# Kernel tuning notes

Measured on AMD Instinct MI355X. Metric: run time of the kernel, lower is better.

## Reference

```python
import jax, jax.numpy as jnp
import numpy as np

EMBED_DIM = 512
NUM_HEADS = 16
TGT_LEN = 1024
BSZ = 4
HEAD_DIM = EMBED_DIM // NUM_HEADS


def setup_inputs() -> dict:
    key = jax.random.key(0)
    ks = jax.random.split(key, 12)
    E = EMBED_DIM
    s = 1.0 / np.sqrt(E)
    query = jax.random.normal(ks[0], (TGT_LEN, BSZ, E), dtype=jnp.float32)
    attn_bias = jax.random.normal(ks[1], (BSZ * NUM_HEADS, TGT_LEN, TGT_LEN), dtype=jnp.float32)
    key_padding_mask = jax.random.randint(ks[2], (BSZ, TGT_LEN), 0, 2) == 1
    q_w = jax.random.normal(ks[3], (E, E), dtype=jnp.float32) * s
    q_b = jax.random.normal(ks[4], (E,), dtype=jnp.float32) * 0.02
    k_w = jax.random.normal(ks[5], (E, E), dtype=jnp.float32) * s
    k_b = jax.random.normal(ks[6], (E,), dtype=jnp.float32) * 0.02
    v_w = jax.random.normal(ks[7], (E, E), dtype=jnp.float32) * s
    v_b = jax.random.normal(ks[8], (E,), dtype=jnp.float32) * 0.02
    out_w = jax.random.normal(ks[9], (E, E), dtype=jnp.float32) * s
    out_b = jax.random.normal(ks[10], (E,), dtype=jnp.float32) * 0.02
    return {
        "query": query, "attn_bias": attn_bias, "key_padding_mask": key_padding_mask,
        "q_w": q_w, "q_b": q_b, "k_w": k_w, "k_b": k_b,
        "v_w": v_w, "v_b": v_b, "out_w": out_w, "out_b": out_b,
    }


def reference(query, attn_bias, key_padding_mask, q_w, q_b, k_w, k_b, v_w, v_b, out_w, out_b):
    Tlen, B, E = query.shape
    H, hd = NUM_HEADS, HEAD_DIM
    scaling = hd ** -0.5
    # self-attention: q/k/v all from query (Linear uses y = x @ W.T + b)
    q = (query @ q_w.T + q_b) * scaling
    k = query @ k_w.T + k_b
    v = query @ v_w.T + v_b
    # [T, B, E] -> [B*H, T, hd]
    q = q.reshape(Tlen, B * H, hd).transpose(1, 0, 2)
    k = k.reshape(Tlen, B * H, hd).transpose(1, 0, 2)
    v = v.reshape(Tlen, B * H, hd).transpose(1, 0, 2)
    # scores [B*H, T, S]
    aw = jnp.einsum('bth,bsh->bts', q, k) + attn_bias
    # key padding mask: [B, S] -> broadcast over heads and tgt
    aw = aw.reshape(B, H, Tlen, Tlen)
    aw = jnp.where(key_padding_mask[:, None, None, :], -jnp.inf, aw)
    aw = aw.reshape(B * H, Tlen, Tlen)
    probs = jax.nn.softmax(aw.astype(jnp.float32), axis=-1)
    attn = jnp.einsum('bts,bsh->bth', probs.astype(query.dtype), v)
    attn = attn.transpose(1, 0, 2).reshape(Tlen, B, E)
    out = attn @ out_w.T + out_b
    # need_weights=True, need_head_weights=False -> mean over heads, [B, T, S]
    attn_weights_avg = probs.reshape(B, H, Tlen, Tlen).mean(axis=1)
    return out, attn_weights_avg
```

## Files before the change

### kernel.cpp

```cpp
#include <hip/hip_runtime.h>
#include <math.h>

typedef __bf16 bf16x8 __attribute__((ext_vector_type(8)));
typedef __bf16 bf16x4 __attribute__((ext_vector_type(4)));
typedef float  f32x4  __attribute__((ext_vector_type(4)));

__global__ __launch_bounds__(256)
void cvt_w(const float* __restrict__ w0, const float* __restrict__ w1,
           const float* __restrict__ w2, const float* __restrict__ w3,
           __bf16* __restrict__ d0, __bf16* __restrict__ d1,
           __bf16* __restrict__ d2, __bf16* __restrict__ d3)
{
    const int y = blockIdx.y;
    const float* s = (y == 0) ? w0 : (y == 1) ? w1 : (y == 2) ? w2 : w3;
    __bf16*      d = (y == 0) ? d0 : (y == 1) ? d1 : (y == 2) ? d2 : d3;
    const int i = blockIdx.x * 256 + threadIdx.x;
    float4 a = *(const float4*)(s + (size_t)i * 8);
    float4 b = *(const float4*)(s + (size_t)i * 8 + 4);
    bf16x8 v;
    v[0] = (__bf16)a.x; v[1] = (__bf16)a.y; v[2] = (__bf16)a.z; v[3] = (__bf16)a.w;
    v[4] = (__bf16)b.x; v[5] = (__bf16)b.y; v[6] = (__bf16)b.z; v[7] = (__bf16)b.w;
    *(bf16x8*)(d + (size_t)i * 8) = v;
}

__global__ __launch_bounds__(256, 2)
void qkv_proj(const float* __restrict__ X,
              const __bf16* __restrict__ Wqb, const __bf16* __restrict__ Wkb,
              const __bf16* __restrict__ Wvb,
              const float* __restrict__ bq, const float* __restrict__ bk,
              const float* __restrict__ bv,
              __bf16* __restrict__ qTb, __bf16* __restrict__ kTb,
              __bf16* __restrict__ vTb)
{
    const int tid  = threadIdx.x;
    const int w    = tid >> 6;
    const int lane = tid & 63;
    const int lq   = lane & 15;
    const int quad = lane >> 4;
    const int n0    = blockIdx.x * 64 + (w >> 1) * 32;
    const int obase = blockIdx.y * 128 + (w & 1) * 64;

    const __bf16* const Wz[3] = { Wqb, Wkb, Wvb };

    f32x4 acc[3][2][4] = {};
    for (int k0 = 0; k0 < 512; k0 += 32) {
        bf16x8 af[2];
#pragma unroll
        for (int m = 0; m < 2; m++) {
            const float* xp = X + (size_t)(n0 + m * 16 + lq) * 512 + k0 + quad * 8;
            float4 x0 = *(const float4*)xp;
            float4 x1 = *(const float4*)(xp + 4);
            bf16x8 v;
            v[0] = (__bf16)x0.x; v[1] = (__bf16)x0.y; v[2] = (__bf16)x0.z; v[3] = (__bf16)x0.w;
            v[4] = (__bf16)x1.x; v[5] = (__bf16)x1.y; v[6] = (__bf16)x1.z; v[7] = (__bf16)x1.w;
            af[m] = v;
        }
#pragma unroll
        for (int z = 0; z < 3; z++) {
            bf16x8 bfr[4];
#pragma unroll
            for (int nn = 0; nn < 4; nn++)
                bfr[nn] = *(const bf16x8*)(Wz[z] + (size_t)(obase + nn * 16 + lq) * 512 + k0 + quad * 8);
#pragma unroll
            for (int m = 0; m < 2; m++)
#pragma unroll
                for (int nn = 0; nn < 4; nn++)
                    acc[z][m][nn] = __builtin_amdgcn_mfma_f32_16x16x32_bf16(af[m], bfr[nn], acc[z][m][nn], 0, 0, 0);
        }
    }

    const float* const ba[3] = { bq, bk, bv };
    const float scaling = 0.17677669529663687f;
#pragma unroll
    for (int z = 0; z < 3; z++)
#pragma unroll
        for (int m = 0; m < 2; m++)
#pragma unroll
            for (int nn = 0; nn < 4; nn++)
#pragma unroll
                for (int r = 0; r < 4; r++) {
                    const int n = n0 + m * 16 + quad * 4 + r;
                    const int o = obase + nn * 16 + lq;
                    float val = acc[z][m][nn][r] + ba[z][o];
                    const int t = n >> 2, b = n & 3;
                    const int h = o >> 5, d = o & 31;
                    const int bh = b * 16 + h;
                    if (z == 0)
                        qTb[(((size_t)bh * 1024 + t) << 5) + d] = (__bf16)(val * scaling);
                    else if (z == 1)
                        kTb[(((size_t)bh * 1024 + t) << 5) + d] = (__bf16)val;
                    else
                        vTb[(((size_t)bh * 32 + d) << 10) + t] = (__bf16)val;
                }
}

__global__ __launch_bounds__(256)
void out_proj(const __bf16* __restrict__ A, const __bf16* __restrict__ Wb,
              const float* __restrict__ bias, float* __restrict__ out,
              float* __restrict__ avg, const __bf16* __restrict__ p1)
{
    if (blockIdx.y >= 4) {
        const size_t i = ((size_t)((blockIdx.y - 4) * 64 + blockIdx.x) * 256 +
                          threadIdx.x) * 8;
        bf16x8 a = *(const bf16x8*)(p1 + i);
        float4 lo = *(float4*)(avg + i);
        float4 hi = *(float4*)(avg + i + 4);
        lo.x += (float)a[0]; lo.y += (float)a[1];
        lo.z += (float)a[2]; lo.w += (float)a[3];
        hi.x += (float)a[4]; hi.y += (float)a[5];
        hi.z += (float)a[6]; hi.w += (float)a[7];
        *(float4*)(avg + i)     = lo;
        *(float4*)(avg + i + 4) = hi;
        return;
    }

    const int tid  = threadIdx.x;
    const int w    = tid >> 6;
    const int lane = tid & 63;
    const int lq   = lane & 15;
    const int quad = lane >> 4;
    const int n0    = blockIdx.x * 64 + (w >> 1) * 32;
    const int obase = blockIdx.y * 128 + (w & 1) * 64;

    f32x4 acc[2][4] = {};
    for (int k0 = 0; k0 < 512; k0 += 32) {
        bf16x8 af[2], bfr[4];
#pragma unroll
        for (int m = 0; m < 2; m++)
            af[m] = *(const bf16x8*)(A + (size_t)(n0 + m * 16 + lq) * 512 + k0 + quad * 8);
#pragma unroll
        for (int nn = 0; nn < 4; nn++)
            bfr[nn] = *(const bf16x8*)(Wb + (size_t)(obase + nn * 16 + lq) * 512 + k0 + quad * 8);
#pragma unroll
        for (int m = 0; m < 2; m++)
#pragma unroll
            for (int nn = 0; nn < 4; nn++)
                acc[m][nn] = __builtin_amdgcn_mfma_f32_16x16x32_bf16(af[m], bfr[nn], acc[m][nn], 0, 0, 0);
    }
#pragma unroll
    for (int m = 0; m < 2; m++)
#pragma unroll
        for (int nn = 0; nn < 4; nn++)
#pragma unroll
            for (int r = 0; r < 4; r++) {
                const int n = n0 + m * 16 + quad * 4 + r;
                const int o = obase + nn * 16 + lq;
                out[(size_t)n * 512 + o] = acc[m][nn][r] + bias[o];
            }
}

__global__ __attribute__((amdgpu_waves_per_eu(2, 2))) __launch_bounds__(512)
void attn_mfma(const __bf16* __restrict__ qTb, const __bf16* __restrict__ kTb,
               const __bf16* __restrict__ vTb, const float* __restrict__ bias,
               const int* __restrict__ mask, __bf16* __restrict__ attnb,
               float* __restrict__ avgf, __bf16* __restrict__ p1)
{
    __shared__ float smem[20800];
    float* const Op0  = smem;
    float* const red0 = &smem[8448];
    __bf16* const Pbase = (__bf16*)&smem[8704];

    const int tid  = threadIdx.x;
    const int w    = tid >> 6;
    const int lane = tid & 63;
    const int lq   = lane & 15;
    const int quad = lane >> 4;

    const int bid = blockIdx.z * 128 + blockIdx.y * 32 + blockIdx.x;
    const int swz = (bid & 7) * 32 + (bid >> 3);
    const int t0  = (swz & 31) * 32;
    const int b   = (swz >> 5) & 3;
    const int z   = swz >> 7;
    const int sbase = w * 128;

    __bf16* const Pw = Pbase + w * 2176;

    unsigned mbits = 0;
    {
        const int* mp = mask + b * 1024 + sbase + quad * 4;
#pragma unroll
        for (int j = 0; j < 8; j++) {
            int4 m4 = *(const int4*)(mp + j * 16);
            mbits |= (unsigned)(m4.x != 0) << (j * 4 + 0);
            mbits |= (unsigned)(m4.y != 0) << (j * 4 + 1);
            mbits |= (unsigned)(m4.z != 0) << (j * 4 + 2);
            mbits |= (unsigned)(m4.w != 0) << (j * 4 + 3);
        }
    }

    const float* const bb = bias + (((size_t)(b * 16 + z * 8)) << 20) +
                            (((size_t)(t0 + lq)) << 10) + sbase + quad * 4;
    const __bf16* const qp0 = qTb + (((size_t)((b * 16 + z * 8) * 1024 + t0)) << 5) +
                              lq * 32 + quad * 8;
    const __bf16* const kp0 = kTb + ((size_t)(b * 16 + z * 8) << 15);
    const __bf16* const vp0 = vTb + ((size_t)(b * 16 + z * 8) << 15);

    bf16x8 qa = *(const bf16x8*)qp0;
    f32x4 cj[8];
#pragma unroll
    for (int j = 0; j < 8; j++) cj[j] = *(const f32x4*)(bb + j * 16);

    float avg0[32] = {}, avg1[32] = {};
    bf16x8 kb[8];
    bf16x8 v0r[4], v1r[4];

    auto body = [&](int hh, int ts, float (&avg)[32]) {
        float* const Op  = Op0  + ts * 4224;
        float* const red = red0 + ts * 128;

        if (ts == 0) {
            const __bf16* kp = kp0 + ((size_t)hh << 15);
            const __bf16* vp = vp0 + ((size_t)hh << 15);
#pragma unroll
            for (int j = 0; j < 8; j++)
                kb[j] = *(const bf16x8*)(kp + (size_t)(sbase + j * 16 + lq) * 32 + quad * 8);
#pragma unroll
            for (int ks = 0; ks < 4; ks++) {
                v0r[ks] = *(const bf16x8*)(vp + (size_t)lq * 1024 + sbase + ks * 32 + quad * 8);
                v1r[ks] = *(const bf16x8*)(vp + (size_t)(16 + lq) * 1024 + sbase + ks * 32 + quad * 8);
            }
        }
        __builtin_amdgcn_sched_barrier(0);

        f32x4 acc[8];
#pragma unroll
        for (int j = 0; j < 8; j++)
            acc[j] = __builtin_amdgcn_mfma_f32_16x16x32_bf16(kb[j], qa, cj[j], 0, 0, 0);
        __builtin_amdgcn_sched_barrier(0);

        {
            const int hn  = (ts == 0) ? hh : ((hh + 1) & 7);
            const int tsn = ts ^ 1;
            qa = *(const bf16x8*)(qp0 + ((size_t)hn << 15) + (tsn << 9));
            const float* bn = bb + ((size_t)hn << 20) + (tsn << 14);
#pragma unroll
            for (int j = 0; j < 8; j++) cj[j] = *(const f32x4*)(bn + j * 16);
        }
        __builtin_amdgcn_sched_barrier(0);

        float sm = 0.f;
#pragma unroll
        for (int j = 0; j < 8; j++)
#pragma unroll
            for (int r = 0; r < 4; r++) {
                float p = __expf(acc[j][r]);
                p = ((mbits >> (j * 4 + r)) & 1u) ? 0.f : p;
                acc[j][r] = p;
                sm += p;
            }
        sm += __shfl_xor(sm, 16);
        sm += __shfl_xor(sm, 32);

#pragma unroll
        for (int j = 0; j < 8; j++) {
            bf16x4 pv;
            pv[0] = (__bf16)acc[j][0]; pv[1] = (__bf16)acc[j][1];
            pv[2] = (__bf16)acc[j][2]; pv[3] = (__bf16)acc[j][3];
            *(bf16x4*)&Pw[lq * 136 + j * 16 + quad * 4] = pv;
        }
        if (lane < 16) red[w * 16 + lane] = sm;

        f32x4 o0 = {0.f, 0.f, 0.f, 0.f}, o1 = {0.f, 0.f, 0.f, 0.f};
#pragma unroll
        for (int ks = 0; ks < 4; ks++) {
            bf16x8 pa = *(const bf16x8*)&Pw[lq * 136 + ks * 32 + quad * 8];
            o0 = __builtin_amdgcn_mfma_f32_16x16x32_bf16(pa, v0r[ks], o0, 0, 0, 0);
            o1 = __builtin_amdgcn_mfma_f32_16x16x32_bf16(pa, v1r[ks], o1, 0, 0, 0);
        }
#pragma unroll
        for (int r = 0; r < 4; r++) {
            Op[w * 528 + (quad * 4 + r) * 33 + lq]      = o0[r];
            Op[w * 528 + (quad * 4 + r) * 33 + 16 + lq] = o1[r];
        }

        __builtin_amdgcn_sched_barrier(0);
        asm volatile("s_waitcnt lgkmcnt(0)" ::: "memory");
        __builtin_amdgcn_s_barrier();
        __builtin_amdgcn_sched_barrier(0);

        {
            const int t = tid >> 5, d = tid & 31;
            float s = 0.f, o = 0.f;
#pragma unroll
            for (int w2 = 0; w2 < 8; w2++) s += red[w2 * 16 + t];
#pragma unroll
            for (int w2 = 0; w2 < 8; w2++) o += Op[w2 * 528 + t * 33 + d];
            attnb[((size_t)(t0 + ts * 16 + t) * 4 + b) * 512 + (z * 8 + hh) * 32 + d] =
                (__bf16)(o / s);
        }

        float s_all = 0.f;
#pragma unroll
        for (int w2 = 0; w2 < 8; w2++) s_all += red[w2 * 16 + lq];
        const float inv = 1.0f / s_all;
#pragma unroll
        for (int j = 0; j < 8; j++) {
            bf16x4 pb = *(const bf16x4*)&Pw[lq * 136 + j * 16 + quad * 4];
#pragma unroll
            for (int r = 0; r < 4; r++)
                avg[j * 4 + r] += (float)pb[r] * inv;
        }
    };

    for (int hh = 0; hh < 8; hh++) {
        body(hh, 0, avg0);
        body(hh, 1, avg1);
    }

#pragma unroll
    for (int ts = 0; ts < 2; ts++) {
        const float* avg = ts ? avg1 : avg0;
        const size_t rowbase = ((size_t)(b * 1024 + t0 + ts * 16 + lq) << 10) +
                               sbase + quad * 4;
        if (z == 0) {
            float* ap = avgf + rowbase;
#pragma unroll
            for (int j = 0; j < 8; j++) {
                f32x4 v = { avg[j * 4 + 0] * 0.0625f, avg[j * 4 + 1] * 0.0625f,
                            avg[j * 4 + 2] * 0.0625f, avg[j * 4 + 3] * 0.0625f };
                *(f32x4*)(ap + j * 16) = v;
            }
        } else {
            __bf16* pp = p1 + rowbase;
#pragma unroll
            for (int j = 0; j < 8; j++) {
                bf16x4 v;
                v[0] = (__bf16)(avg[j * 4 + 0] * 0.0625f);
                v[1] = (__bf16)(avg[j * 4 + 1] * 0.0625f);
                v[2] = (__bf16)(avg[j * 4 + 2] * 0.0625f);
                v[3] = (__bf16)(avg[j * 4 + 3] * 0.0625f);
                *(bf16x4*)(pp + j * 16) = v;
            }
        }
    }
}

extern "C" void kernel_launch(void* const* d_in, const int* in_sizes, int n_in,
                              void* d_out, int out_size, void* d_ws, size_t ws_size,
                              hipStream_t stream)
{
    const float* query     = (const float*)d_in[0];
    const float* attn_bias = (const float*)d_in[1];
    const int*   mask      = (const int*)d_in[2];
    const float* q_w       = (const float*)d_in[3];
    const float* q_b       = (const float*)d_in[4];
    const float* k_w       = (const float*)d_in[5];
    const float* k_b       = (const float*)d_in[6];
    const float* v_w       = (const float*)d_in[7];
    const float* v_b       = (const float*)d_in[8];
    const float* out_w     = (const float*)d_in[9];
    const float* out_b     = (const float*)d_in[10];

    float* out     = (float*)d_out;
    float* avg_out = out + (size_t)2097152;

    char* wsb = (char*)d_ws;
    __bf16* Wqb   = (__bf16*)(wsb);
    __bf16* Wkb   = (__bf16*)(wsb + ((size_t)512 << 10));
    __bf16* Wvb   = (__bf16*)(wsb + ((size_t)1 << 20));
    __bf16* Wob   = (__bf16*)(wsb + ((size_t)1 << 20) + ((size_t)512 << 10));
    __bf16* qTb   = (__bf16*)(wsb + ((size_t)2  << 20));
    __bf16* kTb   = (__bf16*)(wsb + ((size_t)6  << 20));
    __bf16* vTb   = (__bf16*)(wsb + ((size_t)10 << 20));
    __bf16* attnb = (__bf16*)(wsb + ((size_t)14 << 20));
    __bf16* p1    = (__bf16*)(wsb + ((size_t)18 << 20));

    cvt_w<<<dim3(128, 4), dim3(256), 0, stream>>>(
        q_w, k_w, v_w, out_w, Wqb, Wkb, Wvb, Wob);

    qkv_proj<<<dim3(64, 4), dim3(256), 0, stream>>>(
        query, Wqb, Wkb, Wvb, q_b, k_b, v_b, qTb, kTb, vTb);

    attn_mfma<<<dim3(32, 4, 2), dim3(512), 0, stream>>>(
        qTb, kTb, vTb, attn_bias, mask, attnb, avg_out, p1);

    out_proj<<<dim3(64, 36), dim3(256), 0, stream>>>(
        attnb, Wob, out_b, out, avg_out, p1);
}
```

Before: 141.4 us.

## Restructure attention kernel to 4 waves per 16-row tile, two key chunks per wave

The attention kernel now launches 512 blocks of 256 threads. Each block covers 16 query rows instead of 32, and each wave handles 256 keys as two 128-key chunks. K and V fragments are reloaded per chunk rather than held across two row tiles. Shared memory shrinks and the waves_per_eu pin is removed, aiming for more resident blocks and better latency hiding. The cost is twice as many K/V loads per output row and a longer serial chain within each wave.

New measurement: 155.9 us. +10.2%, slower.

```diff
diff --git a/kernel.cpp b/kernel.cpp
--- a/kernel.cpp
+++ b/kernel.cpp
@@ -149,16 +149,16 @@
             }
 }
 
-__global__ __attribute__((amdgpu_waves_per_eu(2, 2))) __launch_bounds__(512)
+__global__ __launch_bounds__(256)
 void attn_mfma(const __bf16* __restrict__ qTb, const __bf16* __restrict__ kTb,
                const __bf16* __restrict__ vTb, const float* __restrict__ bias,
                const int* __restrict__ mask, __bf16* __restrict__ attnb,
                float* __restrict__ avgf, __bf16* __restrict__ p1)
 {
-    __shared__ float smem[20800];
+    __shared__ float smem[12800];
     float* const Op0  = smem;
-    float* const red0 = &smem[8448];
-    __bf16* const Pbase = (__bf16*)&smem[8704];
+    float* const red0 = &smem[4224];
+    __bf16* const Pbase = (__bf16*)&smem[4352];
 
     const int tid  = threadIdx.x;
     const int w    = tid >> 6;
@@ -166,25 +166,33 @@
     const int lq   = lane & 15;
     const int quad = lane >> 4;
 
-    const int bid = blockIdx.z * 128 + blockIdx.y * 32 + blockIdx.x;
-    const int swz = (bid & 7) * 32 + (bid >> 3);
-    const int t0  = (swz & 31) * 32;
-    const int b   = (swz >> 5) & 3;
-    const int z   = swz >> 7;
-    const int sbase = w * 128;
-
-    __bf16* const Pw = Pbase + w * 2176;
-
-    unsigned mbits = 0;
+    const int bid = blockIdx.z * 256 + blockIdx.y * 64 + blockIdx.x;
+    const int swz = (bid & 7) * 64 + (bid >> 3);
+    const int t0  = (swz & 63) * 16;
+    const int b   = (swz >> 6) & 3;
+    const int z   = swz >> 8;
+    const int sbase = w * 256;
+
+    __bf16* const Pw = Pbase + w * 4224;
+
+    unsigned mb0 = 0, mb1 = 0;
     {
         const int* mp = mask + b * 1024 + sbase + quad * 4;
 #pragma unroll
         for (int j = 0; j < 8; j++) {
             int4 m4 = *(const int4*)(mp + j * 16);
-            mbits |= (unsigned)(m4.x != 0) << (j * 4 + 0);
-            mbits |= (unsigned)(m4.y != 0) << (j * 4 + 1);
-            mbits |= (unsigned)(m4.z != 0) << (j * 4 + 2);
-            mbits |= (unsigned)(m4.w != 0) << (j * 4 + 3);
+            mb0 |= (unsigned)(m4.x != 0) << (j * 4 + 0);
+            mb0 |= (unsigned)(m4.y != 0) << (j * 4 + 1);
+            mb0 |= (unsigned)(m4.z != 0) << (j * 4 + 2);
+            mb0 |= (unsigned)(m4.w != 0) << (j * 4 + 3);
+        }
+#pragma unroll
+        for (int j = 0; j < 8; j++) {
+            int4 m4 = *(const int4*)(mp + 128 + j * 16);
+            mb1 |= (unsigned)(m4.x != 0) << (j * 4 + 0);
+            mb1 |= (unsigned)(m4.y != 0) << (j * 4 + 1);
+            mb1 |= (unsigned)(m4.z != 0) << (j * 4 + 2);
+            mb1 |= (unsigned)(m4.w != 0) << (j * 4 + 3);
         }
     }
 
@@ -200,73 +208,86 @@
 #pragma unroll
     for (int j = 0; j < 8; j++) cj[j] = *(const f32x4*)(bb + j * 16);
 
-    float avg0[32] = {}, avg1[32] = {};
-    bf16x8 kb[8];
-    bf16x8 v0r[4], v1r[4];
-
-    auto body = [&](int hh, int ts, float (&avg)[32]) {
-        float* const Op  = Op0  + ts * 4224;
-        float* const red = red0 + ts * 128;
-
-        if (ts == 0) {
-            const __bf16* kp = kp0 + ((size_t)hh << 15);
-            const __bf16* vp = vp0 + ((size_t)hh << 15);
+    float avgc[2][32] = {};
+
+    for (int hh = 0; hh < 8; hh++) {
+        float* const Op  = Op0  + (hh & 1) * 2112;
+        float* const red = red0 + (hh & 1) * 64;
+        const __bf16* kp = kp0 + ((size_t)hh << 15);
+        const __bf16* vp = vp0 + ((size_t)hh << 15);
+
+        float sm = 0.f;
+        f32x4 o0 = {0.f, 0.f, 0.f, 0.f}, o1 = {0.f, 0.f, 0.f, 0.f};
+
+        auto chunk = [&](int c) {
+            const int cb = sbase + c * 128;
+            const unsigned mbits = c ? mb1 : mb0;
+
+            bf16x8 kb[8];
 #pragma unroll
             for (int j = 0; j < 8; j++)
-                kb[j] = *(const bf16x8*)(kp + (size_t)(sbase + j * 16 + lq) * 32 + quad * 8);
+                kb[j] = *(const bf16x8*)(kp + (size_t)(cb + j * 16 + lq) * 32 + quad * 8);
+            bf16x8 v0r[4], v1r[4];
 #pragma unroll
             for (int ks = 0; ks < 4; ks++) {
-                v0r[ks] = *(const bf16x8*)(vp + (size_t)lq * 1024 + sbase + ks * 32 + quad * 8);
-                v1r[ks] = *(const bf16x8*)(vp + (size_t)(16 + lq) * 1024 + sbase + ks * 32 + quad * 8);
-            }
-        }
-        __builtin_amdgcn_sched_barrier(0);
-
-        f32x4 acc[8];
-#pragma unroll
-        for (int j = 0; j < 8; j++)
-            acc[j] = __builtin_amdgcn_mfma_f32_16x16x32_bf16(kb[j], qa, cj[j], 0, 0, 0);
-        __builtin_amdgcn_sched_barrier(0);
-
-        {
-            const int hn  = (ts == 0) ? hh : ((hh + 1) & 7);
-            const int tsn = ts ^ 1;
-            qa = *(const bf16x8*)(qp0 + ((size_t)hn << 15) + (tsn << 9));
-            const float* bn = bb + ((size_t)hn << 20) + (tsn << 14);
-#pragma unroll
-            for (int j = 0; j < 8; j++) cj[j] = *(const f32x4*)(bn + j * 16);
-        }
-        __builtin_amdgcn_sched_barrier(0);
-
-        float sm = 0.f;
-#pragma unroll
-        for (int j = 0; j < 8; j++)
-#pragma unroll
-            for (int r = 0; r < 4; r++) {
-                float p = __expf(acc[j][r]);
-                p = ((mbits >> (j * 4 + r)) & 1u) ? 0.f : p;
-                acc[j][r] = p;
-                sm += p;
-            }
+                v0r[ks] = *(const bf16x8*)(vp + (size_t)lq * 1024 + cb + ks * 32 + quad * 8);
+                v1r[ks] = *(const bf16x8*)(vp + (size_t)(16 + lq) * 1024 + cb + ks * 32 + quad * 8);
+            }
+            __builtin_amdgcn_sched_barrier(0);
+
+            f32x4 acc[8];
+#pragma unroll
+            for (int j = 0; j < 8; j++)
+                acc[j] = __builtin_amdgcn_mfma_f32_16x16x32_bf16(kb[j], qa, cj[j], 0, 0, 0);
+            __builtin_amdgcn_sched_barrier(0);
+
+            {
+                if (c == 0) {
+                    const float* bn = bb + 128;
+#pragma unroll
+                    for (int j = 0; j < 8; j++) cj[j] = *(const f32x4*)(bn + ((size_t)hh << 20) + j * 16);
+                } else {
+                    const int hn = (hh + 1) & 7;
+                    qa = *(const bf16x8*)(qp0 + ((size_t)hn << 15));
+                    const float* bn = bb + ((size_t)hn << 20);
+#pragma unroll
+                    for (int j = 0; j < 8; j++) cj[j] = *(const f32x4*)(bn + j * 16);
+                }
+            }
+            __builtin_amdgcn_sched_barrier(0);
+
+#pragma unroll
+            for (int j = 0; j < 8; j++)
+#pragma unroll
+                for (int r = 0; r < 4; r++) {
+                    float p = __expf(acc[j][r]);
+                    p = ((mbits >> (j * 4 + r)) & 1u) ? 0.f : p;
+                    acc[j][r] = p;
+                    sm += p;
+                }
+
+#pragma unroll
+            for (int j = 0; j < 8; j++) {
+                bf16x4 pv;
+                pv[0] = (__bf16)acc[j][0]; pv[1] = (__bf16)acc[j][1];
+                pv[2] = (__bf16)acc[j][2]; pv[3] = (__bf16)acc[j][3];
+                *(bf16x4*)&Pw[lq * 264 + c * 128 + j * 16 + quad * 4] = pv;
+            }
+
+#pragma unroll
+            for (int ks = 0; ks < 4; ks++) {
+                bf16x8 pa = *(const bf16x8*)&Pw[lq * 264 + c * 128 + ks * 32 + quad * 8];
+                o0 = __builtin_amdgcn_mfma_f32_16x16x32_bf16(pa, v0r[ks], o0, 0, 0, 0);
+                o1 = __builtin_amdgcn_mfma_f32_16x16x32_bf16(pa, v1r[ks], o1, 0, 0, 0);
+            }
+        };
+
+        chunk(0);
+        chunk(1);
+
         sm += __shfl_xor(sm, 16);
         sm += __shfl_xor(sm, 32);
-
-#pragma unroll
-        for (int j = 0; j < 8; j++) {
-            bf16x4 pv;
-            pv[0] = (__bf16)acc[j][0]; pv[1] = (__bf16)acc[j][1];
-            pv[2] = (__bf16)acc[j][2]; pv[3] = (__bf16)acc[j][3];
-            *(bf16x4*)&Pw[lq * 136 + j * 16 + quad * 4] = pv;
-        }
         if (lane < 16) red[w * 16 + lane] = sm;
-
-        f32x4 o0 = {0.f, 0.f, 0.f, 0.f}, o1 = {0.f, 0.f, 0.f, 0.f};
-#pragma unroll
-        for (int ks = 0; ks < 4; ks++) {
-            bf16x8 pa = *(const bf16x8*)&Pw[lq * 136 + ks * 32 + quad * 8];
-            o0 = __builtin_amdgcn_mfma_f32_16x16x32_bf16(pa, v0r[ks], o0, 0, 0, 0);
-            o1 = __builtin_amdgcn_mfma_f32_16x16x32_bf16(pa, v1r[ks], o1, 0, 0, 0);
-        }
 #pragma unroll
         for (int r = 0; r < 4; r++) {
             Op[w * 528 + (quad * 4 + r) * 33 + lq]      = o0[r];
@@ -278,60 +299,58 @@
         __builtin_amdgcn_s_barrier();
         __builtin_amdgcn_sched_barrier(0);
 
-        {
-            const int t = tid >> 5, d = tid & 31;
+#pragma unroll
+        for (int rep = 0; rep < 2; rep++) {
+            const int idx = rep * 256 + tid;
+            const int t = idx >> 5, d = idx & 31;
             float s = 0.f, o = 0.f;
 #pragma unroll
-            for (int w2 = 0; w2 < 8; w2++) s += red[w2 * 16 + t];
-#pragma unroll
-            for (int w2 = 0; w2 < 8; w2++) o += Op[w2 * 528 + t * 33 + d];
-            attnb[((size_t)(t0 + ts * 16 + t) * 4 + b) * 512 + (z * 8 + hh) * 32 + d] =
+            for (int w2 = 0; w2 < 4; w2++) s += red[w2 * 16 + t];
+#pragma unroll
+            for (int w2 = 0; w2 < 4; w2++) o += Op[w2 * 528 + t * 33 + d];
+            attnb[((size_t)(t0 + t) * 4 + b) * 512 + (z * 8 + hh) * 32 + d] =
                 (__bf16)(o / s);
         }
 
         float s_all = 0.f;
 #pragma unroll
-        for (int w2 = 0; w2 < 8; w2++) s_all += red[w2 * 16 + lq];
+        for (int w2 = 0; w2 < 4; w2++) s_all += red[w2 * 16 + lq];
         const float inv = 1.0f / s_all;
 #pragma unroll
-        for (int j = 0; j < 8; j++) {
-            bf16x4 pb = *(const bf16x4*)&Pw[lq * 136 + j * 16 + quad * 4];
-#pragma unroll
-            for (int r = 0; r < 4; r++)
-                avg[j * 4 + r] += (float)pb[r] * inv;
-        }
-    };
-
-    for (int hh = 0; hh < 8; hh++) {
-        body(hh, 0, avg0);
-        body(hh, 1, avg1);
-    }
-
-#pragma unroll
-    for (int ts = 0; ts < 2; ts++) {
-        const float* avg = ts ? avg1 : avg0;
-        const size_t rowbase = ((size_t)(b * 1024 + t0 + ts * 16 + lq) << 10) +
-                               sbase + quad * 4;
-        if (z == 0) {
-            float* ap = avgf + rowbase;
+        for (int c = 0; c < 2; c++)
 #pragma unroll
             for (int j = 0; j < 8; j++) {
-                f32x4 v = { avg[j * 4 + 0] * 0.0625f, avg[j * 4 + 1] * 0.0625f,
-                            avg[j * 4 + 2] * 0.0625f, avg[j * 4 + 3] * 0.0625f };
-                *(f32x4*)(ap + j * 16) = v;
-            }
-        } else {
-            __bf16* pp = p1 + rowbase;
+                bf16x4 pb = *(const bf16x4*)&Pw[lq * 264 + c * 128 + j * 16 + quad * 4];
+#pragma unroll
+                for (int r = 0; r < 4; r++)
+                    avgc[c][j * 4 + r] += (float)pb[r] * inv;
+            }
+    }
+
+    const size_t rowbase = ((size_t)(b * 1024 + t0 + lq) << 10) + sbase + quad * 4;
+    if (z == 0) {
+        float* ap = avgf + rowbase;
+#pragma unroll
+        for (int c = 0; c < 2; c++)
+#pragma unroll
+            for (int j = 0; j < 8; j++) {
+                f32x4 v = { avgc[c][j * 4 + 0] * 0.0625f, avgc[c][j * 4 + 1] * 0.0625f,
+                            avgc[c][j * 4 + 2] * 0.0625f, avgc[c][j * 4 + 3] * 0.0625f };
+                *(f32x4*)(ap + c * 128 + j * 16) = v;
+            }
+    } else {
+        __bf16* pp = p1 + rowbase;
+#pragma unroll
+        for (int c = 0; c < 2; c++)
 #pragma unroll
             for (int j = 0; j < 8; j++) {
                 bf16x4 v;
-                v[0] = (__bf16)(avg[j * 4 + 0] * 0.0625f);
-                v[1] = (__bf16)(avg[j * 4 + 1] * 0.0625f);
-                v[2] = (__bf16)(avg[j * 4 + 2] * 0.0625f);
-                v[3] = (__bf16)(avg[j * 4 + 3] * 0.0625f);
-                *(bf16x4*)(pp + j * 16) = v;
-            }
-        }
+                v[0] = (__bf16)(avgc[c][j * 4 + 0] * 0.0625f);
+                v[1] = (__bf16)(avgc[c][j * 4 + 1] * 0.0625f);
+                v[2] = (__bf16)(avgc[c][j * 4 + 2] * 0.0625f);
+                v[3] = (__bf16)(avgc[c][j * 4 + 3] * 0.0625f);
+                *(bf16x4*)(pp + c * 128 + j * 16) = v;
+            }
     }
 }
 
@@ -371,7 +390,7 @@
     qkv_proj<<<dim3(64, 4), dim3(256), 0, stream>>>(
         query, Wqb, Wkb, Wvb, q_b, k_b, v_b, qTb, kTb, vTb);
 
-    attn_mfma<<<dim3(32, 4, 2), dim3(512), 0, stream>>>(
+    attn_mfma<<<dim3(64, 4, 2), dim3(256), 0, stream>>>(
         qTb, kTb, vTb, attn_bias, mask, attnb, avg_out, p1);
 
     out_proj<<<dim3(64, 36), dim3(256), 0, stream>>>(
```
